# Kernel tuning notes

Hardware: AMD Instinct MI355X
Metric: run time of the kernel (lower is better)

## Reference

```python
import jax, jax.numpy as jnp
import numpy as np

DECAY = 0.95

def setup_inputs() -> dict:
    key = jax.random.key(0)
    k1, k2, k3, k4 = jax.random.split(key, 4)
    B, S, H, Dk, Dv = 4, 4096, 16, 64, 64
    return {
        "memory": jax.random.normal(k1, (H, Dk, Dv), dtype=jnp.float32),
        "keys": jax.random.normal(k2, (B, S, H, Dk), dtype=jnp.float32),
        "values": jax.random.normal(k3, (B, S, H, Dv), dtype=jnp.float32),
        "write_strengths": jax.random.uniform(k4, (B, S), dtype=jnp.float32),
    }

def reference(memory, keys, values, write_strengths):
    # M_new = decay * M + sum_{b,s} rho[b,s] * k[b,s,h] v[b,s,h]^T
    # Algebraically equivalent to per-head (rho-weighted) K^T V contraction;
    # avoids materializing the (B,S,H,Dk,Dv) outer-product tensor.
    delta = jnp.einsum('bs,bshk,bshv->hkv', write_strengths, keys, values)
    return DECAY * memory + delta
```

## Files before the change

### kernel.cpp

```cpp
#include <hip/hip_runtime.h>


constexpr int HH = 16;
constexpr int DK = 64;
constexpr int DV = 64;
constexpr int ROWS = 16384;
constexpr int NCHUNK = 64;
constexpr int RPB = ROWS / NCHUNK;
constexpr int TSR = 32;
constexpr int NT = RPB / TSR;
constexpr float DECAY = 0.95f;

__global__ __launch_bounds__(256) void init_out(const float* __restrict__ mem,
                                                float* __restrict__ out) {
    int i = blockIdx.x * 256 + threadIdx.x;
    out[i] = DECAY * mem[i];
}

__device__ __forceinline__ void dma16(const float* g, float* l) {
    __builtin_amdgcn_global_load_lds(
        (const __attribute__((address_space(1))) void*)g,
        (__attribute__((address_space(3))) void*)l, 16, 0, 0);
}

__global__ __launch_bounds__(256) void accum(const float* __restrict__ keys,
                                             const float* __restrict__ values,
                                             const float* __restrict__ rho,
                                             float* __restrict__ out) {
    __shared__ float sK[2][TSR * DK];
    __shared__ float sV[2][TSR * DV];
    __shared__ float sR[RPB];

    const int t    = threadIdx.x;
    const int w    = t >> 6;
    const int lane = t & 63;
    const int tk   = lane >> 3;
    const int tv   = lane & 7;
    const int chunk = blockIdx.x;
    const int h     = blockIdx.y;
    const int row0  = chunk * RPB;

    const int dr = t >> 4;
    const int dc = (t & 15) * 4;

    __builtin_amdgcn_global_load_lds(
        (const __attribute__((address_space(1))) void*)(rho + row0 + t),
        (__attribute__((address_space(3))) void*)(sR + t), 4, 0, 0);

    {
        const float* kg = keys   + ((size_t)(row0 + dr) * HH + h) * DK + dc;
        const float* vg = values + ((size_t)(row0 + dr) * HH + h) * DV + dc;
        dma16(kg, &sK[0][dr * DK + dc]);
        dma16(kg + 16 * HH * DK, &sK[0][(dr + 16) * DK + dc]);
        dma16(vg, &sV[0][dr * DV + dc]);
        dma16(vg + 16 * HH * DV, &sV[0][(dr + 16) * DV + dc]);
    }

    float4 acc[8][2];
    #pragma unroll
    for (int i = 0; i < 8; ++i) {
        acc[i][0] = make_float4(0.f, 0.f, 0.f, 0.f);
        acc[i][1] = make_float4(0.f, 0.f, 0.f, 0.f);
    }

    __syncthreads();

    for (int tile = 0; tile < NT; ++tile) {
        const int cur = tile & 1;
        const int nxt = cur ^ 1;

        if (tile + 1 < NT) {
            const int r = row0 + (tile + 1) * TSR + dr;
            const float* kg = keys   + ((size_t)r * HH + h) * DK + dc;
            const float* vg = values + ((size_t)r * HH + h) * DV + dc;
            dma16(kg, &sK[nxt][dr * DK + dc]);
            dma16(kg + 16 * HH * DK, &sK[nxt][(dr + 16) * DK + dc]);
            dma16(vg, &sV[nxt][dr * DV + dc]);
            dma16(vg + 16 * HH * DV, &sV[nxt][(dr + 16) * DV + dc]);
        }

        const float* kb = &sK[cur][w * 8 * DK];
        const float* vb = &sV[cur][w * 8 * DV];
        const float* rb = &sR[tile * TSR + w * 8];

        #pragma unroll
        for (int si = 0; si < 8; ++si) {
            float4 kf  = *(const float4*)(kb + si * DK + tk * 8);
            float4 kf2 = *(const float4*)(kb + si * DK + tk * 8 + 4);
            float4 vf  = *(const float4*)(vb + si * DV + tv * 8);
            float4 vf2 = *(const float4*)(vb + si * DV + tv * 8 + 4);
            float r = rb[si];
            kf.x *= r; kf.y *= r; kf.z *= r; kf.w *= r;
            kf2.x *= r; kf2.y *= r; kf2.z *= r; kf2.w *= r;

            #define FMA_ROW(I, KV)                                  \
                acc[I][0].x = fmaf(KV, vf.x,  acc[I][0].x);         \
                acc[I][0].y = fmaf(KV, vf.y,  acc[I][0].y);         \
                acc[I][0].z = fmaf(KV, vf.z,  acc[I][0].z);         \
                acc[I][0].w = fmaf(KV, vf.w,  acc[I][0].w);         \
                acc[I][1].x = fmaf(KV, vf2.x, acc[I][1].x);         \
                acc[I][1].y = fmaf(KV, vf2.y, acc[I][1].y);         \
                acc[I][1].z = fmaf(KV, vf2.z, acc[I][1].z);         \
                acc[I][1].w = fmaf(KV, vf2.w, acc[I][1].w);
            FMA_ROW(0, kf.x)  FMA_ROW(1, kf.y)  FMA_ROW(2, kf.z)  FMA_ROW(3, kf.w)
            FMA_ROW(4, kf2.x) FMA_ROW(5, kf2.y) FMA_ROW(6, kf2.z) FMA_ROW(7, kf2.w)
            #undef FMA_ROW
        }

        __syncthreads();
    }

    float* red = (w & 1) ? &sV[0][0] : &sK[0][0];

    if (w < 2) {
        #pragma unroll
        for (int i = 0; i < 8; ++i) {
            *(float4*)(red + (tk * 8 + i) * 64 + tv * 8)     = acc[i][0];
            *(float4*)(red + (tk * 8 + i) * 64 + tv * 8 + 4) = acc[i][1];
        }
    }
    __syncthreads();
    if (w >= 2) {
        #pragma unroll
        for (int i = 0; i < 8; ++i) {
            float4* p0 = (float4*)(red + (tk * 8 + i) * 64 + tv * 8);
            float4* p1 = p0 + 1;
            float4 c0 = *p0, c1 = *p1;
            c0.x += acc[i][0].x; c0.y += acc[i][0].y;
            c0.z += acc[i][0].z; c0.w += acc[i][0].w;
            c1.x += acc[i][1].x; c1.y += acc[i][1].y;
            c1.z += acc[i][1].z; c1.w += acc[i][1].w;
            *p0 = c0; *p1 = c1;
        }
    }
    __syncthreads();

    float* o = out + h * (DK * DV);
    const float* r0 = &sK[0][0];
    const float* r1 = &sV[0][0];
    #pragma unroll
    for (int i = 0; i < 16; ++i) {
        int idx = i * 256 + t;
        atomicAdd(o + idx, r0[idx] + r1[idx]);
    }
}

extern "C" void kernel_launch(void* const* d_in, const int* in_sizes, int n_in,
                              void* d_out, int out_size, void* d_ws, size_t ws_size,
                              hipStream_t stream) {
    const float* mem    = (const float*)d_in[0];
    const float* keys   = (const float*)d_in[1];
    const float* values = (const float*)d_in[2];
    const float* rho    = (const float*)d_in[3];
    float* out = (float*)d_out;

    init_out<<<dim3((HH * DK * DV) / 256), dim3(256), 0, stream>>>(mem, out);

    dim3 grid(NCHUNK, HH);
    accum<<<grid, dim3(256), 0, stream>>>(keys, values, rho, out);
}
```

Baseline: 165.9 us.

## Replace LDS-staged tiles with per-wave direct register loads and padded reduction

Each wave now owns a contiguous slice of rows and loads its key/value fragments straight from global memory into registers, software-pipelined one row ahead. This removes the shared-memory double buffering, the async LDS DMA and the per-tile block barriers. The reduction buffer is padded to 68 floats per row to avoid LDS bank conflicts. The cost is that each lane issues small strided 32-byte global loads that are replicated across lanes (tk and tv overlap) with far less latency hiding, so the kernel relies on caches and occupancy (launch bounds of 4 blocks) to cover memory latency.

```diff
diff --git a/kernel.cpp b/kernel.cpp
--- a/kernel.cpp
+++ b/kernel.cpp
@@ -5,10 +5,11 @@
 constexpr int DK = 64;
 constexpr int DV = 64;
 constexpr int ROWS = 16384;
-constexpr int NCHUNK = 64;
-constexpr int RPB = ROWS / NCHUNK;
-constexpr int TSR = 32;
-constexpr int NT = RPB / TSR;
+constexpr int NSLICE = 64;
+constexpr int RPB = ROWS / NSLICE;
+constexpr int RPW = RPB / 4;
+constexpr int RSTRIDE = HH * DK;
+constexpr int PAD = 68;
 constexpr float DECAY = 0.95f;
 
 __global__ __launch_bounds__(256) void init_out(const float* __restrict__ mem,
@@ -17,44 +18,23 @@
     out[i] = DECAY * mem[i];
 }
 
-__device__ __forceinline__ void dma16(const float* g, float* l) {
-    __builtin_amdgcn_global_load_lds(
-        (const __attribute__((address_space(1))) void*)g,
-        (__attribute__((address_space(3))) void*)l, 16, 0, 0);
-}
-
-__global__ __launch_bounds__(256) void accum(const float* __restrict__ keys,
-                                             const float* __restrict__ values,
-                                             const float* __restrict__ rho,
-                                             float* __restrict__ out) {
-    __shared__ float sK[2][TSR * DK];
-    __shared__ float sV[2][TSR * DV];
-    __shared__ float sR[RPB];
+__global__ __launch_bounds__(256, 4) void accum(const float* __restrict__ keys,
+                                                const float* __restrict__ values,
+                                                const float* __restrict__ rho,
+                                                float* __restrict__ out) {
+    __shared__ float red[2][64 * PAD];
 
     const int t    = threadIdx.x;
     const int w    = t >> 6;
     const int lane = t & 63;
     const int tk   = lane >> 3;
     const int tv   = lane & 7;
-    const int chunk = blockIdx.x;
-    const int h     = blockIdx.y;
-    const int row0  = chunk * RPB;
+    const int h    = blockIdx.y;
+    const int row0 = blockIdx.x * RPB + w * RPW;
 
-    const int dr = t >> 4;
-    const int dc = (t & 15) * 4;
-
-    __builtin_amdgcn_global_load_lds(
-        (const __attribute__((address_space(1))) void*)(rho + row0 + t),
-        (__attribute__((address_space(3))) void*)(sR + t), 4, 0, 0);
-
-    {
-        const float* kg = keys   + ((size_t)(row0 + dr) * HH + h) * DK + dc;
-        const float* vg = values + ((size_t)(row0 + dr) * HH + h) * DV + dc;
-        dma16(kg, &sK[0][dr * DK + dc]);
-        dma16(kg + 16 * HH * DK, &sK[0][(dr + 16) * DK + dc]);
-        dma16(vg, &sV[0][dr * DV + dc]);
-        dma16(vg + 16 * HH * DV, &sV[0][(dr + 16) * DV + dc]);
-    }
+    const float* kp = keys   + ((size_t)row0 * HH + h) * DK + tk * 8;
+    const float* vp = values + ((size_t)row0 * HH + h) * DV + tv * 8;
+    const float* rp = rho + row0;
 
     float4 acc[8][2];
     #pragma unroll
@@ -63,67 +43,63 @@
         acc[i][1] = make_float4(0.f, 0.f, 0.f, 0.f);
     }
 
-    __syncthreads();
+    float4 ck0 = *(const float4*)kp;
+    float4 ck1 = *(const float4*)(kp + 4);
+    float4 cv0 = *(const float4*)vp;
+    float4 cv1 = *(const float4*)(vp + 4);
+    float  cr  = rp[0];
 
-    for (int tile = 0; tile < NT; ++tile) {
-        const int cur = tile & 1;
-        const int nxt = cur ^ 1;
-
-        if (tile + 1 < NT) {
-            const int r = row0 + (tile + 1) * TSR + dr;
-            const float* kg = keys   + ((size_t)r * HH + h) * DK + dc;
-            const float* vg = values + ((size_t)r * HH + h) * DV + dc;
-            dma16(kg, &sK[nxt][dr * DK + dc]);
-            dma16(kg + 16 * HH * DK, &sK[nxt][(dr + 16) * DK + dc]);
-            dma16(vg, &sV[nxt][dr * DV + dc]);
-            dma16(vg + 16 * HH * DV, &sV[nxt][(dr + 16) * DV + dc]);
-        }
-
-        const float* kb = &sK[cur][w * 8 * DK];
-        const float* vb = &sV[cur][w * 8 * DV];
-        const float* rb = &sR[tile * TSR + w * 8];
-
-        #pragma unroll
-        for (int si = 0; si < 8; ++si) {
-            float4 kf  = *(const float4*)(kb + si * DK + tk * 8);
-            float4 kf2 = *(const float4*)(kb + si * DK + tk * 8 + 4);
-            float4 vf  = *(const float4*)(vb + si * DV + tv * 8);
-            float4 vf2 = *(const float4*)(vb + si * DV + tv * 8 + 4);
-            float r = rb[si];
-            kf.x *= r; kf.y *= r; kf.z *= r; kf.w *= r;
-            kf2.x *= r; kf2.y *= r; kf2.z *= r; kf2.w *= r;
-
-            #define FMA_ROW(I, KV)                                  \
-                acc[I][0].x = fmaf(KV, vf.x,  acc[I][0].x);         \
-                acc[I][0].y = fmaf(KV, vf.y,  acc[I][0].y);         \
-                acc[I][0].z = fmaf(KV, vf.z,  acc[I][0].z);         \
-                acc[I][0].w = fmaf(KV, vf.w,  acc[I][0].w);         \
-                acc[I][1].x = fmaf(KV, vf2.x, acc[I][1].x);         \
-                acc[I][1].y = fmaf(KV, vf2.y, acc[I][1].y);         \
-                acc[I][1].z = fmaf(KV, vf2.z, acc[I][1].z);         \
-                acc[I][1].w = fmaf(KV, vf2.w, acc[I][1].w);
-            FMA_ROW(0, kf.x)  FMA_ROW(1, kf.y)  FMA_ROW(2, kf.z)  FMA_ROW(3, kf.w)
-            FMA_ROW(4, kf2.x) FMA_ROW(5, kf2.y) FMA_ROW(6, kf2.z) FMA_ROW(7, kf2.w)
-            #undef FMA_ROW
-        }
-
-        __syncthreads();
+    #define COMPUTE_ROW()                                                   \
+    {                                                                       \
+        float k0 = ck0.x * cr, k1 = ck0.y * cr, k2 = ck0.z * cr,            \
+              k3 = ck0.w * cr, k4 = ck1.x * cr, k5 = ck1.y * cr,            \
+              k6 = ck1.z * cr, k7 = ck1.w * cr;                             \
+        _Pragma("unroll")                                                   \
+        for (int _d = 0; _d < 1; ++_d) {                                    \
+            float kv[8] = {k0, k1, k2, k3, k4, k5, k6, k7};                 \
+            _Pragma("unroll")                                               \
+            for (int i = 0; i < 8; ++i) {                                   \
+                acc[i][0].x = fmaf(kv[i], cv0.x, acc[i][0].x);              \
+                acc[i][0].y = fmaf(kv[i], cv0.y, acc[i][0].y);              \
+                acc[i][0].z = fmaf(kv[i], cv0.z, acc[i][0].z);              \
+                acc[i][0].w = fmaf(kv[i], cv0.w, acc[i][0].w);              \
+                acc[i][1].x = fmaf(kv[i], cv1.x, acc[i][1].x);              \
+                acc[i][1].y = fmaf(kv[i], cv1.y, acc[i][1].y);              \
+                acc[i][1].z = fmaf(kv[i], cv1.z, acc[i][1].z);              \
+                acc[i][1].w = fmaf(kv[i], cv1.w, acc[i][1].w);              \
+            }                                                               \
+        }                                                                   \
     }
 
-    float* red = (w & 1) ? &sV[0][0] : &sK[0][0];
+    for (int r = 0; r < RPW - 1; ++r) {
+        const float* kq = kp + (size_t)(r + 1) * RSTRIDE;
+        const float* vq = vp + (size_t)(r + 1) * RSTRIDE;
+        float4 nk0 = *(const float4*)kq;
+        float4 nk1 = *(const float4*)(kq + 4);
+        float4 nv0 = *(const float4*)vq;
+        float4 nv1 = *(const float4*)(vq + 4);
+        float  nr  = rp[r + 1];
 
+        COMPUTE_ROW();
+
+        ck0 = nk0; ck1 = nk1; cv0 = nv0; cv1 = nv1; cr = nr;
+    }
+    COMPUTE_ROW();
+    #undef COMPUTE_ROW
+
+    float* dst = red[w & 1];
     if (w < 2) {
         #pragma unroll
         for (int i = 0; i < 8; ++i) {
-            *(float4*)(red + (tk * 8 + i) * 64 + tv * 8)     = acc[i][0];
-            *(float4*)(red + (tk * 8 + i) * 64 + tv * 8 + 4) = acc[i][1];
+            *(float4*)(dst + (tk * 8 + i) * PAD + tv * 8)     = acc[i][0];
+            *(float4*)(dst + (tk * 8 + i) * PAD + tv * 8 + 4) = acc[i][1];
         }
     }
     __syncthreads();
     if (w >= 2) {
         #pragma unroll
         for (int i = 0; i < 8; ++i) {
-            float4* p0 = (float4*)(red + (tk * 8 + i) * 64 + tv * 8);
+            float4* p0 = (float4*)(dst + (tk * 8 + i) * PAD + tv * 8);
             float4* p1 = p0 + 1;
             float4 c0 = *p0, c1 = *p1;
             c0.x += acc[i][0].x; c0.y += acc[i][0].y;
@@ -136,12 +112,11 @@
     __syncthreads();
 
     float* o = out + h * (DK * DV);
-    const float* r0 = &sK[0][0];
-    const float* r1 = &sV[0][0];
     #pragma unroll
     for (int i = 0; i < 16; ++i) {
         int idx = i * 256 + t;
-        atomicAdd(o + idx, r0[idx] + r1[idx]);
+        int rr = idx >> 6, cc = idx & 63;
+        atomicAdd(o + idx, red[0][rr * PAD + cc] + red[1][rr * PAD + cc]);
     }
 }
 
@@ -156,6 +131,6 @@
 
     init_out<<<dim3((HH * DK * DV) / 256), dim3(256), 0, stream>>>(mem, out);
 
-    dim3 grid(NCHUNK, HH);
+    dim3 grid(NSLICE, HH);
     accum<<<grid, dim3(256), 0, stream>>>(keys, values, rho, out);
 }
```

Measured after the change: 606.5 us. 265% more time.
